# Kernel optimization log

Measured on AMD Instinct MI355X. Metric: run time of the kernel, lower is better.

## Reference

```python
import jax, jax.numpy as jnp
import numpy as np

B = 131072      # batch of states
N_ACT = 40      # output_dim (Tetris action space)


def setup_inputs() -> dict:
    key = jax.random.key(0)
    ks = jax.random.split(key, 9)
    # state vector: 11 real-valued board features, 1 hold-piece id in [0,4),
    # 3 next-piece ids in [1,8) (0 is treated as invalid by the original code)
    keep = jax.random.normal(ks[0], (B, 11), dtype=jnp.float32)
    hold = jax.random.randint(ks[1], (B, 1), 0, 4).astype(jnp.float32)
    nxt = jax.random.randint(ks[2], (B, 3), 1, 8).astype(jnp.float32)
    x = jnp.concatenate([keep, hold, nxt], axis=1)  # [B, 15]
    W1 = jax.random.normal(ks[3], (36, 128), dtype=jnp.float32) * 0.1
    b1 = jnp.zeros((128,), dtype=jnp.float32)
    W2 = jax.random.normal(ks[4], (128, 512), dtype=jnp.float32) * 0.05
    b2 = jnp.zeros((512,), dtype=jnp.float32)
    W4 = jax.random.normal(ks[5], (512, N_ACT), dtype=jnp.float32) * 0.05
    b4 = jnp.zeros((N_ACT,), dtype=jnp.float32)
    return {"x": x, "W1": W1, "b1": b1, "W2": W2, "b2": b2, "W4": W4, "b4": b4}


def reference(x, W1, b1, W2, b2, W4, b4):
    B_, _ = x.shape
    keep = x[:, :11]                                      # [B, 11]
    # vectorized replacement of the per-sample .item() one-hot loop
    hold_idx = jax.lax.stop_gradient(jnp.clip(x[:, 11].astype(jnp.int32), 0, 3))
    nxt_idx = jax.lax.stop_gradient(jnp.clip(x[:, 12:15].astype(jnp.int32) - 1, 0, 6))
    hold_oh = jax.nn.one_hot(hold_idx, 4, dtype=x.dtype)  # [B, 4]
    nxt_oh = jax.nn.one_hot(nxt_idx, 7, dtype=x.dtype).reshape(B_, 21)  # [B, 21]
    inp = jnp.concatenate([keep, hold_oh, nxt_oh], axis=1)  # [B, 36]
    h = jax.nn.relu(inp @ W1 + b1)   # [B, 128]
    h = jax.nn.relu(h @ W2 + b2)     # [B, 512]
    return h @ W4 + b4               # [B, N_ACT]
```

## Files before the change

### kernel.cpp

```cpp
#include <hip/hip_runtime.h>


typedef short bf16x8 __attribute__((ext_vector_type(8)));
typedef float f32x4 __attribute__((ext_vector_type(4)));
typedef unsigned int u32;

#define NW1F 8192
#define NW2F 65536
#define NW4F 24576
#define PACK_TOTAL (NW1F + NW2F + NW4F)
#define PACK_THREADS (PACK_TOTAL / 8)

__device__ __forceinline__ unsigned short f2bf(float f) {
  union { float f; unsigned u; } a; a.f = f;
  unsigned r = a.u + 0x7fffu + ((a.u >> 16) & 1u);
  return (unsigned short)(r >> 16);
}
__device__ __forceinline__ u32 cvtpk(float lo, float hi) {
  u32 r;
  asm("v_cvt_pk_bf16_f32 %0, %1, %2" : "=v"(r) : "v"(lo), "v"(hi));
  return r;
}

__global__ void pack_weights(const float* __restrict__ W1,
                             const float* __restrict__ W2,
                             const float* __restrict__ W4,
                             unsigned short* __restrict__ wf) {
  int t = blockIdx.x * 256 + threadIdx.x;
  if (t >= PACK_THREADS) return;
  int fid = t >> 6, lane = t & 63;
  int l16 = lane & 15, quad = lane >> 4;
  float vals[8];
  if (fid < 16) {
    int mt = fid >> 1, ks = fid & 1;
    int m = mt * 16 + l16, k0 = ks * 32 + quad * 8;
#pragma unroll
    for (int j = 0; j < 8; ++j) { int k = k0 + j; vals[j] = (k < 36) ? W1[k * 128 + m] : 0.f; }
  } else if (fid < 144) {
    int f = fid - 16, mt = f >> 2, ks = f & 3;
    int m = mt * 16 + l16, k0 = ks * 32 + quad * 8;
#pragma unroll
    for (int j = 0; j < 8; ++j) vals[j] = W2[(k0 + j) * 512 + m];
  } else {
    int f = fid - 144, mt = f >> 4, ks = f & 15;
    int m = mt * 16 + l16, k0 = ks * 32 + quad * 8;
#pragma unroll
    for (int j = 0; j < 8; ++j) vals[j] = (m < 40) ? W4[(k0 + j) * 40 + m] : 0.f;
  }
  u32 p[4];
#pragma unroll
  for (int j = 0; j < 4; ++j) p[j] = cvtpk(vals[2 * j], vals[2 * j + 1]);
  *(bf16x8*)(wf + (size_t)t * 8) = *(bf16x8*)p;
}

__global__ __launch_bounds__(64, 3) void dqn_fused(
    const float* __restrict__ x,
    const unsigned short* __restrict__ wf,
    const float* __restrict__ b1,
    const float* __restrict__ b2,
    const float* __restrict__ b4,
    float* __restrict__ out) {
  __shared__ __align__(16) unsigned short su[32 * 72];

  const int lane = threadIdx.x & 63;
  const int quad = lane >> 4;
  const int l16  = lane & 15;
  const int row0 = blockIdx.x << 5;

  const unsigned short* w2f = wf + NW1F;
  const unsigned short* w4f = wf + NW1F + NW2F;
  const unsigned short* w2p = w2f + lane * 8;

  bf16x8 curW[4];
#pragma unroll
  for (int k = 0; k < 4; ++k) curW[k] = *(const bf16x8*)(w2p + (size_t)k * 512);

  if (lane < 32) {
    const float* xr = x + (size_t)(row0 + lane) * 15;
    unsigned short* dst = su + lane * 72;
    bf16x8 z = {0, 0, 0, 0, 0, 0, 0, 0};
#pragma unroll
    for (int c = 8; c < 64; c += 8) *(bf16x8*)(dst + c) = z;
    u32 p[4];
#pragma unroll
    for (int i = 0; i < 4; ++i) p[i] = cvtpk(xr[2 * i], xr[2 * i + 1]);
    *(bf16x8*)dst = *(bf16x8*)p;
    *(u32*)(dst + 8) = cvtpk(xr[8], xr[9]);
    dst[10] = f2bf(xr[10]);
    int hold = (int)xr[11]; hold = hold < 0 ? 0 : (hold > 3 ? 3 : hold);
    dst[11 + hold] = 0x3F80;
#pragma unroll
    for (int t = 0; t < 3; ++t) {
      int nx = (int)xr[12 + t] - 1; nx = nx < 0 ? 0 : (nx > 6 ? 6 : nx);
      dst[15 + t * 7 + nx] = 0x3F80;
    }
  }

  bf16x8 ib[2][2];
#pragma unroll
  for (int rg = 0; rg < 2; ++rg)
#pragma unroll
    for (int ks = 0; ks < 2; ++ks)
      ib[rg][ks] = *(const bf16x8*)(su + (rg * 16 + l16) * 72 + ks * 32 + quad * 8);

  bf16x8 af1[2][4];
#pragma unroll
  for (int half = 0; half < 2; ++half) {
    bf16x8 wa[4][2];
#pragma unroll
    for (int mtl = 0; mtl < 4; ++mtl)
#pragma unroll
      for (int ks = 0; ks < 2; ++ks)
        wa[mtl][ks] = *(const bf16x8*)(
            wf + (size_t)(((half * 4 + mtl) * 2 + ks) * 64 + lane) * 8);

    f32x4 acc1[4][2];
#pragma unroll
    for (int mtl = 0; mtl < 4; ++mtl) {
      f32x4 bias = *(const f32x4*)(b1 + (half * 4 + mtl) * 16 + quad * 4);
#pragma unroll
      for (int rg = 0; rg < 2; ++rg) acc1[mtl][rg] = bias;
    }
#pragma unroll
    for (int mtl = 0; mtl < 4; ++mtl)
#pragma unroll
      for (int ks = 0; ks < 2; ++ks)
#pragma unroll
        for (int rg = 0; rg < 2; ++rg)
          acc1[mtl][rg] = __builtin_amdgcn_mfma_f32_16x16x32_bf16(wa[mtl][ks], ib[rg][ks], acc1[mtl][rg], 0, 0, 0);

#pragma unroll
    for (int mtl = 0; mtl < 4; ++mtl)
#pragma unroll
      for (int rg = 0; rg < 2; ++rg) {
        float v0 = fmaxf(acc1[mtl][rg][0], 0.f);
        float v1 = fmaxf(acc1[mtl][rg][1], 0.f);
        float v2 = fmaxf(acc1[mtl][rg][2], 0.f);
        float v3 = fmaxf(acc1[mtl][rg][3], 0.f);
        uint2 pk = {cvtpk(v0, v1), cvtpk(v2, v3)};
        *(uint2*)(su + (rg * 16 + l16) * 72 + mtl * 16 + quad * 4) = pk;
      }
#pragma unroll
    for (int rg = 0; rg < 2; ++rg)
#pragma unroll
      for (int ksl = 0; ksl < 2; ++ksl)
        af1[rg][half * 2 + ksl] =
            *(const bf16x8*)(su + (rg * 16 + l16) * 72 + ksl * 32 + quad * 8);
  }

  f32x4 accO[3][2];
#pragma unroll
  for (int mt3 = 0; mt3 < 3; ++mt3) {
    int colbase = mt3 * 16 + quad * 4;
    f32x4 bias = *(const f32x4*)(b4 + (colbase < 40 ? colbase : 36));
#pragma unroll
    for (int rg = 0; rg < 2; ++rg) accO[mt3][rg] = bias;
  }

  for (int chunk = 0; chunk < 8; ++chunk) {
    bf16x8 w4r[2][3];
#pragma unroll
    for (int ks3 = 0; ks3 < 2; ++ks3)
#pragma unroll
      for (int mt3 = 0; mt3 < 3; ++mt3)
        w4r[ks3][mt3] = *(const bf16x8*)(
            w4f + (size_t)((mt3 * 16 + chunk * 2 + ks3) * 64 + lane) * 8);

#pragma unroll
    for (int mtl = 0; mtl < 4; ++mtl) {
      int fb = chunk * 16 + mtl * 4 + 4;
      if (fb >= 128) fb = 0;
      bf16x8 nxtW[4];
#pragma unroll
      for (int k = 0; k < 4; ++k)
        nxtW[k] = *(const bf16x8*)(w2p + (size_t)(fb + k) * 512);

      f32x4 acc2[2];
      f32x4 b2v = *(const f32x4*)(b2 + chunk * 64 + mtl * 16 + quad * 4);
#pragma unroll
      for (int rg = 0; rg < 2; ++rg) acc2[rg] = b2v;
#pragma unroll
      for (int ks = 0; ks < 4; ++ks)
#pragma unroll
        for (int rg = 0; rg < 2; ++rg)
          acc2[rg] = __builtin_amdgcn_mfma_f32_16x16x32_bf16(curW[ks], af1[rg][ks], acc2[rg], 0, 0, 0);

#pragma unroll
      for (int rg = 0; rg < 2; ++rg) {
        float v0 = fmaxf(acc2[rg][0], 0.f);
        float v1 = fmaxf(acc2[rg][1], 0.f);
        float v2 = fmaxf(acc2[rg][2], 0.f);
        float v3 = fmaxf(acc2[rg][3], 0.f);
        uint2 pk = {cvtpk(v0, v1), cvtpk(v2, v3)};
        *(uint2*)(su + (rg * 16 + l16) * 72 + mtl * 16 + quad * 4) = pk;
      }
#pragma unroll
      for (int k = 0; k < 4; ++k) curW[k] = nxtW[k];
    }

#pragma unroll
    for (int ks3 = 0; ks3 < 2; ++ks3) {
      bf16x8 h[2];
#pragma unroll
      for (int rg = 0; rg < 2; ++rg)
        h[rg] = *(const bf16x8*)(su + (rg * 16 + l16) * 72 + ks3 * 32 + quad * 8);
#pragma unroll
      for (int mt3 = 0; mt3 < 3; ++mt3)
#pragma unroll
        for (int rg = 0; rg < 2; ++rg)
          accO[mt3][rg] = __builtin_amdgcn_mfma_f32_16x16x32_bf16(w4r[ks3][mt3], h[rg], accO[mt3][rg], 0, 0, 0);
    }
  }

#pragma unroll
  for (int mt3 = 0; mt3 < 3; ++mt3) {
    int colbase = mt3 * 16 + quad * 4;
    if (colbase < 40) {
#pragma unroll
      for (int rg = 0; rg < 2; ++rg) {
        size_t row = (size_t)(row0 + rg * 16 + l16);
        *(f32x4*)(out + row * 40 + colbase) = accO[mt3][rg];
      }
    }
  }
}

extern "C" void kernel_launch(void* const* d_in, const int* in_sizes, int n_in,
                              void* d_out, int out_size, void* d_ws, size_t ws_size,
                              hipStream_t stream) {
  const float* x  = (const float*)d_in[0];
  const float* W1 = (const float*)d_in[1];
  const float* b1 = (const float*)d_in[2];
  const float* W2 = (const float*)d_in[3];
  const float* b2 = (const float*)d_in[4];
  const float* W4 = (const float*)d_in[5];
  const float* b4 = (const float*)d_in[6];
  float* out = (float*)d_out;
  unsigned short* wf = (unsigned short*)d_ws;

  int B = in_sizes[0] / 15;

  hipLaunchKernelGGL(pack_weights, dim3((PACK_THREADS + 255) / 256), dim3(256), 0, stream,
                     W1, W2, W4, wf);
  hipLaunchKernelGGL(dqn_fused, dim3(B / 32), dim3(64), 0, stream,
                     x, wf, b1, b2, b4, out);
}
```

Measured before the change: 118.8 us.

## Process 64 rows per wavefront and stagger chunk order across blocks

```diff
diff --git a/kernel.cpp b/kernel.cpp
--- a/kernel.cpp
+++ b/kernel.cpp
@@ -3,6 +3,7 @@
 
 typedef short bf16x8 __attribute__((ext_vector_type(8)));
 typedef float f32x4 __attribute__((ext_vector_type(4)));
+typedef float f32x4u __attribute__((ext_vector_type(4), aligned(4)));
 typedef unsigned int u32;
 
 #define NW1F 8192
@@ -53,19 +54,20 @@
   *(bf16x8*)(wf + (size_t)t * 8) = *(bf16x8*)p;
 }
 
-__global__ __launch_bounds__(64, 3) void dqn_fused(
+__global__ __launch_bounds__(64, 2) void dqn_fused(
     const float* __restrict__ x,
     const unsigned short* __restrict__ wf,
     const float* __restrict__ b1,
     const float* __restrict__ b2,
     const float* __restrict__ b4,
     float* __restrict__ out) {
-  __shared__ __align__(16) unsigned short su[32 * 72];
+  __shared__ __align__(16) unsigned short su[64 * 72];
 
   const int lane = threadIdx.x & 63;
   const int quad = lane >> 4;
   const int l16  = lane & 15;
-  const int row0 = blockIdx.x << 5;
+  const int row0 = blockIdx.x << 6;
+  const int base = (blockIdx.x & 3) * 2;
 
   const unsigned short* w2f = wf + NW1F;
   const unsigned short* w4f = wf + NW1F + NW2F;
@@ -73,37 +75,45 @@
 
   bf16x8 curW[4];
 #pragma unroll
-  for (int k = 0; k < 4; ++k) curW[k] = *(const bf16x8*)(w2p + (size_t)k * 512);
-
-  if (lane < 32) {
+  for (int k = 0; k < 4; ++k)
+    curW[k] = *(const bf16x8*)(w2p + (size_t)(base * 16 + k) * 512);
+  f32x4 b2cur[4];
+#pragma unroll
+  for (int mtl = 0; mtl < 4; ++mtl)
+    b2cur[mtl] = *(const f32x4*)(b2 + base * 64 + mtl * 16 + quad * 4);
+
+  {
     const float* xr = x + (size_t)(row0 + lane) * 15;
+    f32x4u q0 = *(const f32x4u*)(xr);
+    f32x4u q1 = *(const f32x4u*)(xr + 4);
+    f32x4u q2 = *(const f32x4u*)(xr + 8);
+    f32x4u q3 = *(const f32x4u*)(xr + 11);
     unsigned short* dst = su + lane * 72;
     bf16x8 z = {0, 0, 0, 0, 0, 0, 0, 0};
 #pragma unroll
     for (int c = 8; c < 64; c += 8) *(bf16x8*)(dst + c) = z;
-    u32 p[4];
-#pragma unroll
-    for (int i = 0; i < 4; ++i) p[i] = cvtpk(xr[2 * i], xr[2 * i + 1]);
+    u32 p[4] = {cvtpk(q0[0], q0[1]), cvtpk(q0[2], q0[3]),
+                cvtpk(q1[0], q1[1]), cvtpk(q1[2], q1[3])};
     *(bf16x8*)dst = *(bf16x8*)p;
-    *(u32*)(dst + 8) = cvtpk(xr[8], xr[9]);
-    dst[10] = f2bf(xr[10]);
-    int hold = (int)xr[11]; hold = hold < 0 ? 0 : (hold > 3 ? 3 : hold);
+    *(u32*)(dst + 8) = cvtpk(q2[0], q2[1]);
+    dst[10] = f2bf(q2[2]);
+    int hold = (int)q3[0]; hold = hold < 0 ? 0 : (hold > 3 ? 3 : hold);
     dst[11 + hold] = 0x3F80;
 #pragma unroll
     for (int t = 0; t < 3; ++t) {
-      int nx = (int)xr[12 + t] - 1; nx = nx < 0 ? 0 : (nx > 6 ? 6 : nx);
+      int nx = (int)q3[1 + t] - 1; nx = nx < 0 ? 0 : (nx > 6 ? 6 : nx);
       dst[15 + t * 7 + nx] = 0x3F80;
     }
   }
 
-  bf16x8 ib[2][2];
-#pragma unroll
-  for (int rg = 0; rg < 2; ++rg)
+  bf16x8 ib[4][2];
+#pragma unroll
+  for (int rg = 0; rg < 4; ++rg)
 #pragma unroll
     for (int ks = 0; ks < 2; ++ks)
       ib[rg][ks] = *(const bf16x8*)(su + (rg * 16 + l16) * 72 + ks * 32 + quad * 8);
 
-  bf16x8 af1[2][4];
+  bf16x8 af1[4][4];
 #pragma unroll
   for (int half = 0; half < 2; ++half) {
     bf16x8 wa[4][2];
@@ -114,25 +124,25 @@
         wa[mtl][ks] = *(const bf16x8*)(
             wf + (size_t)(((half * 4 + mtl) * 2 + ks) * 64 + lane) * 8);
 
-    f32x4 acc1[4][2];
+    f32x4 acc1[4][4];
 #pragma unroll
     for (int mtl = 0; mtl < 4; ++mtl) {
       f32x4 bias = *(const f32x4*)(b1 + (half * 4 + mtl) * 16 + quad * 4);
 #pragma unroll
-      for (int rg = 0; rg < 2; ++rg) acc1[mtl][rg] = bias;
+      for (int rg = 0; rg < 4; ++rg) acc1[mtl][rg] = bias;
     }
 #pragma unroll
     for (int mtl = 0; mtl < 4; ++mtl)
 #pragma unroll
       for (int ks = 0; ks < 2; ++ks)
 #pragma unroll
-        for (int rg = 0; rg < 2; ++rg)
+        for (int rg = 0; rg < 4; ++rg)
           acc1[mtl][rg] = __builtin_amdgcn_mfma_f32_16x16x32_bf16(wa[mtl][ks], ib[rg][ks], acc1[mtl][rg], 0, 0, 0);
 
 #pragma unroll
     for (int mtl = 0; mtl < 4; ++mtl)
 #pragma unroll
-      for (int rg = 0; rg < 2; ++rg) {
+      for (int rg = 0; rg < 4; ++rg) {
         float v0 = fmaxf(acc1[mtl][rg][0], 0.f);
         float v1 = fmaxf(acc1[mtl][rg][1], 0.f);
         float v2 = fmaxf(acc1[mtl][rg][2], 0.f);
@@ -141,23 +151,31 @@
         *(uint2*)(su + (rg * 16 + l16) * 72 + mtl * 16 + quad * 4) = pk;
       }
 #pragma unroll
-    for (int rg = 0; rg < 2; ++rg)
+    for (int rg = 0; rg < 4; ++rg)
 #pragma unroll
       for (int ksl = 0; ksl < 2; ++ksl)
         af1[rg][half * 2 + ksl] =
             *(const bf16x8*)(su + (rg * 16 + l16) * 72 + ksl * 32 + quad * 8);
   }
 
-  f32x4 accO[3][2];
+  f32x4 accO[3][4];
 #pragma unroll
   for (int mt3 = 0; mt3 < 3; ++mt3) {
     int colbase = mt3 * 16 + quad * 4;
     f32x4 bias = *(const f32x4*)(b4 + (colbase < 40 ? colbase : 36));
 #pragma unroll
-    for (int rg = 0; rg < 2; ++rg) accO[mt3][rg] = bias;
-  }
-
-  for (int chunk = 0; chunk < 8; ++chunk) {
+    for (int rg = 0; rg < 4; ++rg) accO[mt3][rg] = bias;
+  }
+
+  for (int i = 0; i < 8; ++i) {
+    const int chunk  = (base + i) & 7;
+    const int chunkN = (base + i + 1) & 7;
+
+    f32x4 b2nxt[4];
+#pragma unroll
+    for (int mtl = 0; mtl < 4; ++mtl)
+      b2nxt[mtl] = *(const f32x4*)(b2 + chunkN * 64 + mtl * 16 + quad * 4);
+
     bf16x8 w4r[2][3];
 #pragma unroll
     for (int ks3 = 0; ks3 < 2; ++ks3)
@@ -168,25 +186,23 @@
 
 #pragma unroll
     for (int mtl = 0; mtl < 4; ++mtl) {
-      int fb = chunk * 16 + mtl * 4 + 4;
-      if (fb >= 128) fb = 0;
+      const int fb = (mtl < 3) ? (chunk * 16 + (mtl + 1) * 4) : (chunkN * 16);
       bf16x8 nxtW[4];
 #pragma unroll
       for (int k = 0; k < 4; ++k)
         nxtW[k] = *(const bf16x8*)(w2p + (size_t)(fb + k) * 512);
 
-      f32x4 acc2[2];
-      f32x4 b2v = *(const f32x4*)(b2 + chunk * 64 + mtl * 16 + quad * 4);
-#pragma unroll
-      for (int rg = 0; rg < 2; ++rg) acc2[rg] = b2v;
+      f32x4 acc2[4];
+#pragma unroll
+      for (int rg = 0; rg < 4; ++rg) acc2[rg] = b2cur[mtl];
 #pragma unroll
       for (int ks = 0; ks < 4; ++ks)
 #pragma unroll
-        for (int rg = 0; rg < 2; ++rg)
+        for (int rg = 0; rg < 4; ++rg)
           acc2[rg] = __builtin_amdgcn_mfma_f32_16x16x32_bf16(curW[ks], af1[rg][ks], acc2[rg], 0, 0, 0);
 
 #pragma unroll
-      for (int rg = 0; rg < 2; ++rg) {
+      for (int rg = 0; rg < 4; ++rg) {
         float v0 = fmaxf(acc2[rg][0], 0.f);
         float v1 = fmaxf(acc2[rg][1], 0.f);
         float v2 = fmaxf(acc2[rg][2], 0.f);
@@ -200,16 +216,18 @@
 
 #pragma unroll
     for (int ks3 = 0; ks3 < 2; ++ks3) {
-      bf16x8 h[2];
-#pragma unroll
-      for (int rg = 0; rg < 2; ++rg)
+      bf16x8 h[4];
+#pragma unroll
+      for (int rg = 0; rg < 4; ++rg)
         h[rg] = *(const bf16x8*)(su + (rg * 16 + l16) * 72 + ks3 * 32 + quad * 8);
 #pragma unroll
       for (int mt3 = 0; mt3 < 3; ++mt3)
 #pragma unroll
-        for (int rg = 0; rg < 2; ++rg)
+        for (int rg = 0; rg < 4; ++rg)
           accO[mt3][rg] = __builtin_amdgcn_mfma_f32_16x16x32_bf16(w4r[ks3][mt3], h[rg], accO[mt3][rg], 0, 0, 0);
     }
+#pragma unroll
+    for (int mtl = 0; mtl < 4; ++mtl) b2cur[mtl] = b2nxt[mtl];
   }
 
 #pragma unroll
@@ -217,7 +235,7 @@
     int colbase = mt3 * 16 + quad * 4;
     if (colbase < 40) {
 #pragma unroll
-      for (int rg = 0; rg < 2; ++rg) {
+      for (int rg = 0; rg < 4; ++rg) {
         size_t row = (size_t)(row0 + rg * 16 + l16);
         *(f32x4*)(out + row * 40 + colbase) = accO[mt3][rg];
       }
@@ -242,6 +260,6 @@
 
   hipLaunchKernelGGL(pack_weights, dim3((PACK_THREADS + 255) / 256), dim3(256), 0, stream,
                      W1, W2, W4, wf);
-  hipLaunchKernelGGL(dqn_fused, dim3(B / 32), dim3(64), 0, stream,
+  hipLaunchKernelGGL(dqn_fused, dim3(B / 64), dim3(64), 0, stream,
                      x, wf, b1, b2, b4, out);
 }
```

After: 109.2 us. 1.09x faster.
